# Kernel optimization log

Hardware: AMD Instinct MI355X
Metric: run time of the kernel (lower is better)

The kernel has to match this reference:

```python
import jax, jax.numpy as jnp
import numpy as np

N_NODES = 5000
K_POOL = 30
BN_EPS = 1e-5


def setup_inputs() -> dict:
    key = jax.random.key(0)
    ks = jax.random.split(key, 16)
    B, N, Din, C, H, OUT, E = 32, N_NODES, 16, 64, 128, 2, 80000
    F_tot = Din + 3 * C  # concat of input + 3 conv layers = 208
    return {
        "x": jax.random.normal(ks[0], (B, N, Din), jnp.float32),
        "age": jax.random.uniform(ks[1], (B,), jnp.float32) * 100.0,
        "edge_attr": jax.random.uniform(ks[2], (E,), jnp.float32) + 0.1,
        "W0": jax.random.normal(ks[3], (Din, C), jnp.float32) * 0.1,
        "b0": jnp.zeros((C,), jnp.float32),
        "W1": jax.random.normal(ks[4], (C, C), jnp.float32) * 0.1,
        "b1": jnp.zeros((C,), jnp.float32),
        "W2": jax.random.normal(ks[5], (C, C), jnp.float32) * 0.1,
        "b2": jnp.zeros((C,), jnp.float32),
        "g0": jnp.ones((C,), jnp.float32),
        "be0": jnp.zeros((C,), jnp.float32),
        "g1": jnp.ones((C,), jnp.float32),
        "be1": jnp.zeros((C,), jnp.float32),
        "mW0": jax.random.normal(ks[6], (K_POOL * F_tot + 1, H), jnp.float32) * 0.02,
        "mb0": jnp.zeros((H,), jnp.float32),
        "mW1": jax.random.normal(ks[7], (H, OUT), jnp.float32) * 0.1,
        "mb1": jnp.zeros((OUT,), jnp.float32),
        "edge_row": jax.random.randint(ks[8], (E,), 0, N, jnp.int32),
        "edge_col": jax.random.randint(ks[9], (E,), 0, N, jnp.int32),
    }


def _spmm(xw, rows, cols, nv):
    # xw: (B, N, C); out[b, r] = sum_{edges (r,c)} nv * xw[b, c]
    def one(xb):
        return jax.ops.segment_sum(xb[cols] * nv[:, None], rows, num_segments=N_NODES)
    return jax.vmap(one)(xw)


def reference(x, age, edge_attr, W0, b0, W1, b1, W2, b2, g0, be0, g1, be1,
              mW0, mb0, mW1, mb1, edge_row, edge_col):
    N = N_NODES
    # GCN normalization on A + I (gcn_norm with edge weights, self-loop value 1)
    loop = jnp.arange(N, dtype=edge_row.dtype)
    rows = jnp.concatenate([edge_row, loop])
    cols = jnp.concatenate([edge_col, loop])
    vals = jnp.concatenate([edge_attr, jnp.ones((N,), edge_attr.dtype)])
    deg = jax.ops.segment_sum(vals, rows, num_segments=N)
    dinv = jnp.where(deg > 0, jax.lax.rsqrt(jnp.maximum(deg, 1e-12)), 0.0)
    nv = dinv[rows] * vals * dinv[cols]

    feats = [x]
    h = x
    convs = [(W0, b0), (W1, b1), (W2, b2)]
    bns = [(g0, be0), (g1, be1)]
    for i, (W, b) in enumerate(convs):
        h = _spmm(h @ W, rows, cols, nv) + b  # GCNConv
        if i < len(convs) - 1:
            g, be = bns[i]
            mu = jnp.mean(h, axis=(0, 1))   # BatchNorm1d over flattened (B*N, C)
            var = jnp.var(h, axis=(0, 1))
            h = (h - mu) * jax.lax.rsqrt(var + BN_EPS) * g + be
        h = jax.nn.relu(h)  # dropout p=0.0 -> identity
        feats.append(h)

    z = jnp.concatenate(feats, axis=-1)  # (B, N, 208)
    # global_sort_pool: sort nodes by last feature channel, descending, take top-k
    order = jnp.argsort(-z[:, :, -1], axis=1)[:, :K_POOL]  # (B, k)
    zk = jnp.take_along_axis(z, order[:, :, None], axis=1)  # (B, k, 208)
    flat = zk.reshape(z.shape[0], -1)
    flat = jnp.concatenate([flat, age[:, None]], axis=1)  # append age scalar

    hm = jax.nn.relu(flat @ mW0 + mb0)  # MLP head
    out = hm @ mW1 + mb1
    return jax.nn.log_softmax(out, axis=-1)
```

## Files before the change

kernel.cpp:

```cpp
#include <hip/hip_runtime.h>
#include <math.h>

#define NN    5000
#define NE    80000
#define NB    32
#define DIN   16
#define CH    64
#define KPOOL 30
#define FTOT  208
#define FLATW 6241
#define NH    128
#define NG    8
#define GB    4
#define NPB   16
#define NCHUNK 313
#define NPAD  5008
#define NEPAD (NE + 4 * NN)
#define NSLOT 32



__global__ void k_init(float* deg, int* counts, float* stats, float* hm, int* perm) {
    int i = blockIdx.x * 256 + threadIdx.x;
    if (i < NN) { deg[i] = 1.0f; counts[i] = 0; }
    if (i < 2 * NSLOT * 128) stats[i] = 0.0f;
    if (i < 4096) hm[i] = 0.0f;
    if (i >= NN && i < NPAD) perm[i] = NN;
}

#define NEB 313
__global__ void k_edges(const float* __restrict__ attr, const int* __restrict__ erow,
                        float* deg, int* counts) {
    int e = blockIdx.x * 256 + threadIdx.x;
    if (e < NE) {
        int r = erow[e];
        atomicAdd(&deg[r], attr[e]);
        atomicAdd(&counts[r], 1);
    }
}

__global__ __launch_bounds__(1024) void k_phase1(
        const int* __restrict__ counts, const float* __restrict__ deg,
        int* rowptr, int* cursor, float* dinv, int* perm,
        const float* __restrict__ x, float* __restrict__ xt) {
    __shared__ int wsum[16], woff[16];
    __shared__ int carry_sh;
    __shared__ int hist[256];
    int t = threadIdx.x;
    if (blockIdx.x >= 2) {
        int idx = (blockIdx.x - 2) * 1024 + t;
        if (idx >= NB * NN) return;
        int b = idx / NN, n = idx % NN;
        int g4 = b >> 3, bi8 = b & 7;
        const float4* src = (const float4*)(x + (size_t)idx * DIN);
        float4* dst = (float4*)(xt + (((size_t)g4 * NN + n) * 8 + bi8) * DIN);
        dst[0] = src[0]; dst[1] = src[1]; dst[2] = src[2]; dst[3] = src[3];
        return;
    }
    if (blockIdx.x == 0) {
        int lane = t & 63, wid = t >> 6;
        if (t == 0) carry_sh = 0;
        __syncthreads();
        for (int base = 0; base < NN; base += 1024) {
            int carry = carry_sh;
            int i = base + t;
            int v = 0;
            if (i < NN) {
                v = (counts[i] + 3) & ~3;
                dinv[i] = 1.0f / sqrtf(deg[i]);
            }
            int s = v;
#pragma unroll
            for (int off = 1; off < 64; off <<= 1) {
                int o = __shfl_up(s, off);
                if (lane >= off) s += o;
            }
            if (lane == 63) wsum[wid] = s;
            __syncthreads();
            if (t < 16) {
                int w = wsum[t];
#pragma unroll
                for (int off = 1; off < 16; off <<= 1) {
                    int o = __shfl_up(w, off);
                    if (t >= off) w += o;
                }
                woff[t] = w;
            }
            __syncthreads();
            int inc = s + (wid > 0 ? woff[wid - 1] : 0) + carry;
            if (i < NN) {
                rowptr[i + 1] = inc;
                cursor[i] = inc - v;
            }
            if (t == 1023) carry_sh = carry + woff[15];
            __syncthreads();
        }
        if (t == 0) rowptr[0] = 0;
    } else {
        if (t < 256) hist[t] = 0;
        __syncthreads();
        for (int i = t; i < NN; i += 1024) {
            int b = 255 - min(((counts[i] + 3) & ~3) >> 2, 255);
            atomicAdd(&hist[b], 1);
        }
        __syncthreads();
        int mycnt = (t < 256) ? hist[t] : 0;
        for (int off = 1; off < 256; off <<= 1) {
            int v = (t < 256 && t >= off) ? hist[t - off] : 0;
            __syncthreads();
            if (t < 256) hist[t] += v;
            __syncthreads();
        }
        if (t < 256) hist[t] -= mycnt;
        __syncthreads();
        for (int i = t; i < NN; i += 1024) {
            int b = 255 - min(((counts[i] + 3) & ~3) >> 2, 255);
            int pos = atomicAdd(&hist[b], 1);
            perm[pos] = i;
        }
    }
}

__global__ __launch_bounds__(1024) void k_build(
        const int* __restrict__ erow, const int* __restrict__ ecol,
        const float* __restrict__ attr, const float* __restrict__ dinv,
        const int* __restrict__ counts, const int* __restrict__ rowptr,
        int* cursor, int* csr_col, float* csr_nv) {
    int t = blockIdx.x * 1024 + threadIdx.x;
    if (t < NE) {
        int r = erow[t], c = ecol[t];
        int pos = atomicAdd(&cursor[r], 1);
        csr_col[pos] = c;
        csr_nv[pos] = dinv[r] * attr[t] * dinv[c];
    } else if (t - NE < NN) {
        int i = t - NE;
        int cnt = counts[i];
        int pcnt = (cnt + 3) & ~3;
        int base = rowptr[i + 1] - pcnt;
        for (int p = base + cnt; p < base + pcnt; ++p) { csr_col[p] = i; csr_nv[p] = 0.0f; }
    }
}

__device__ __forceinline__ float4 actv(float4 v, float4 s, float4 t) {
    v.x = fmaxf(fmaf(v.x, s.x, t.x), 0.f);
    v.y = fmaxf(fmaf(v.y, s.y, t.y), 0.f);
    v.z = fmaxf(fmaf(v.z, s.z, t.z), 0.f);
    v.w = fmaxf(fmaf(v.w, s.w, t.w), 0.f);
    return v;
}
__device__ __forceinline__ void fma4(float4& a, float w, float4 v) {
    a.x = fmaf(w, v.x, a.x); a.y = fmaf(w, v.y, a.y);
    a.z = fmaf(w, v.z, a.z); a.w = fmaf(w, v.w, a.w);
}
__device__ __forceinline__ void fma2(float2& a, float w, float2 v) {
    a.x = fmaf(w, v.x, a.x); a.y = fmaf(w, v.y, a.y);
}

__global__ __launch_bounds__(256) void k_l16(
        const float* __restrict__ in,
        const float* __restrict__ W, const float* __restrict__ bias,
        const int* __restrict__ rowptr, const int* __restrict__ csr_col,
        const float* __restrict__ csr_nv, const float* __restrict__ dinv,
        const int* __restrict__ perm,
        float* __restrict__ out, float* __restrict__ stats) {
    const int ALS = 18;
    __shared__ float As[4 * 32 * ALS];
    int tid = threadIdx.x;
    int wid = tid >> 6, lane = tid & 63;
    int g4 = blockIdx.x & 3;
    int base = (blockIdx.x >> 2) * NPB + wid * 4;
    float* Aw = As + wid * 32 * ALS;
    const int4 pid = *(const int4*)(perm + base);

    const float2* __restrict__ in2 = (const float2*)in + (size_t)g4 * NN * 64;
    int bi8 = lane >> 3, chp = lane & 7;

#pragma unroll
    for (int pr = 0; pr < 2; ++pr) {
        int id0 = (pr == 0) ? pid.x : pid.z;
        int id1 = (pr == 0) ? pid.y : pid.w;
        bool vn0 = id0 < NN, vn1 = id1 < NN;
        int rc0 = vn0 ? id0 : 0, rc1 = vn1 ? id1 : 0;
        float dd0 = dinv[rc0]; dd0 *= dd0;
        float dd1 = dinv[rc1]; dd1 *= dd1;
        float2 a0 = {0.f, 0.f}, a1 = {0.f, 0.f};
        {
            float2 v0 = in2[(size_t)rc0 * 64 + lane];
            float2 v1 = in2[(size_t)rc1 * 64 + lane];
            if (vn0) { a0.x = dd0 * v0.x; a0.y = dd0 * v0.y; }
            if (vn1) { a1.x = dd1 * v1.x; a1.y = dd1 * v1.y; }
        }
        int p0a = rowptr[rc0], na = vn0 ? (rowptr[rc0 + 1] - p0a) >> 2 : 0;
        int p0b = rowptr[rc1], nbv = vn1 ? (rowptr[rc1 + 1] - p0b) >> 2 : 0;
        int mx = max(na, nbv);
        for (int bb = 0; bb < mx; ++bb) {
            int ea = min(p0a + 4 * bb, NEPAD - 4);
            int eb = min(p0b + 4 * bb, NEPAD - 4);
            bool va = bb < na, vb = bb < nbv;
            int4   ca = *(const int4*)(csr_col + ea);
            float4 wa = *(const float4*)(csr_nv + ea);
            int4   cb = *(const int4*)(csr_col + eb);
            float4 wb = *(const float4*)(csr_nv + eb);
            if (!va) { wa.x = 0.f; wa.y = 0.f; wa.z = 0.f; wa.w = 0.f;
                       ca.x = 0; ca.y = 0; ca.z = 0; ca.w = 0; }
            if (!vb) { wb.x = 0.f; wb.y = 0.f; wb.z = 0.f; wb.w = 0.f;
                       cb.x = 0; cb.y = 0; cb.z = 0; cb.w = 0; }
            float2 u0 = in2[(size_t)ca.x * 64 + lane];
            float2 u1 = in2[(size_t)ca.y * 64 + lane];
            float2 u2 = in2[(size_t)ca.z * 64 + lane];
            float2 u3 = in2[(size_t)ca.w * 64 + lane];
            float2 t0 = in2[(size_t)cb.x * 64 + lane];
            float2 t1 = in2[(size_t)cb.y * 64 + lane];
            float2 t2 = in2[(size_t)cb.z * 64 + lane];
            float2 t3 = in2[(size_t)cb.w * 64 + lane];
            fma2(a0, wa.x, u0);
            fma2(a0, wa.y, u1);
            fma2(a0, wa.z, u2);
            fma2(a0, wa.w, u3);
            fma2(a1, wb.x, t0);
            fma2(a1, wb.y, t1);
            fma2(a1, wb.z, t2);
            fma2(a1, wb.w, t3);
        }
        *(float2*)(Aw + ((2 * pr + 0) * 8 + bi8) * ALS + chp * 2) = a0;
        *(float2*)(Aw + ((2 * pr + 1) * 8 + bi8) * ALS + chp * 2) = a1;
    }

    int colq = lane & 15, rowq = lane >> 4;
    int node = (rowq == 0) ? pid.x : (rowq == 1) ? pid.y : (rowq == 2) ? pid.z : pid.w;

    const float4* __restrict__ W4 = (const float4*)W;
    float4 bb4 = ((const float4*)bias)[colq];
    float4 o[8];
#pragma unroll
    for (int i = 0; i < 8; ++i) o[i] = bb4;
#pragma unroll
    for (int k = 0; k < 16; ++k) {
        float4 w4 = W4[k * 16 + colq];
#pragma unroll
        for (int i = 0; i < 8; ++i)
            fma4(o[i], Aw[(rowq * 8 + i) * ALS + k], w4);
    }
    if (node < NN) {
#pragma unroll
        for (int i = 0; i < 8; ++i) {
            int g8 = g4 * 2 + (i >> 2);
            float4* op = (float4*)(out + (((size_t)g8 * NN + node) * 4 + (i & 3)) * 64);
            op[colq] = o[i];
        }
    }

    float4 s4 = {0,0,0,0}, q4 = {0,0,0,0};
    if (node < NN) {
#pragma unroll
        for (int i = 0; i < 8; ++i) {
            s4.x += o[i].x; s4.y += o[i].y; s4.z += o[i].z; s4.w += o[i].w;
            q4.x = fmaf(o[i].x, o[i].x, q4.x); q4.y = fmaf(o[i].y, o[i].y, q4.y);
            q4.z = fmaf(o[i].z, o[i].z, q4.z); q4.w = fmaf(o[i].w, o[i].w, q4.w);
        }
    }
    s4.x += __shfl_xor(s4.x, 16); s4.y += __shfl_xor(s4.y, 16);
    s4.z += __shfl_xor(s4.z, 16); s4.w += __shfl_xor(s4.w, 16);
    q4.x += __shfl_xor(q4.x, 16); q4.y += __shfl_xor(q4.y, 16);
    q4.z += __shfl_xor(q4.z, 16); q4.w += __shfl_xor(q4.w, 16);
    s4.x += __shfl_xor(s4.x, 32); s4.y += __shfl_xor(s4.y, 32);
    s4.z += __shfl_xor(s4.z, 32); s4.w += __shfl_xor(s4.w, 32);
    q4.x += __shfl_xor(q4.x, 32); q4.y += __shfl_xor(q4.y, 32);
    q4.z += __shfl_xor(q4.z, 32); q4.w += __shfl_xor(q4.w, 32);
    __syncthreads();
    if (lane < 16) {
        float* S = As + wid * 128;
        *(float4*)(S + lane * 8) = s4;
        *(float4*)(S + lane * 8 + 4) = q4;
    }
    __syncthreads();
    if (tid < 64) {
        int cq = tid >> 2, comp = tid & 3;
        float s = 0.f, q = 0.f;
#pragma unroll
        for (int w = 0; w < 4; ++w) {
            s += As[w * 128 + cq * 8 + comp];
            q += As[w * 128 + cq * 8 + 4 + comp];
        }
        float* sl = stats + (blockIdx.x & (NSLOT - 1)) * 128;
        atomicAdd(&sl[tid], s);
        atomicAdd(&sl[64 + tid], q);
    }
}

__global__ __launch_bounds__(256) void k_l64(
        const float* __restrict__ in, const float* __restrict__ bnstats,
        const float* __restrict__ gamma, const float* __restrict__ beta,
        const float* __restrict__ W, const float* __restrict__ bias,
        const int* __restrict__ rowptr, const int* __restrict__ csr_col,
        const float* __restrict__ csr_nv, const float* __restrict__ dinv,
        const int* __restrict__ perm,
        float* __restrict__ out, float* __restrict__ stats) {
    const int ALS = 68;
    __shared__ float As[4 * 16 * ALS];
    __shared__ float stl[128];
    int tid = threadIdx.x;
    int wid = tid >> 6, lane = tid & 63;
    int g = blockIdx.x & 7;
    int base = (blockIdx.x >> 3) * NPB + wid * 4;
    float* Aw = As + wid * 16 * ALS;
    const int4 pid = *(const int4*)(perm + base);

    if (tid < 64) {
        float su = 0.f, qu = 0.f;
#pragma unroll
        for (int s = 0; s < NSLOT; ++s) {
            su += bnstats[s * 128 + tid];
            qu += bnstats[s * 128 + 64 + tid];
        }
        const float inv = 1.0f / (float)(NB * NN);
        float mu = su * inv;
        float var = qu * inv - mu * mu;
        float sc = gamma[tid] / sqrtf(var + 1e-5f);
        stl[tid] = sc;
        stl[64 + tid] = fmaf(-mu, sc, beta[tid]);
    }
    __syncthreads();

    const float4* __restrict__ in4 = (const float4*)in + (size_t)g * NN * 64;
    int c4 = lane & 15, bi = lane >> 4;
    float4 sv = ((const float4*)stl)[c4];
    float4 tv = ((const float4*)(stl + 64))[c4];
#pragma unroll
    for (int pr = 0; pr < 2; ++pr) {
        int id0 = (pr == 0) ? pid.x : pid.z;
        int id1 = (pr == 0) ? pid.y : pid.w;
        bool vn0 = id0 < NN, vn1 = id1 < NN;
        int rc0 = vn0 ? id0 : 0, rc1 = vn1 ? id1 : 0;
        float dd0 = dinv[rc0]; dd0 *= dd0;
        float dd1 = dinv[rc1]; dd1 *= dd1;
        float4 a0 = {0.f,0.f,0.f,0.f}, a1 = {0.f,0.f,0.f,0.f};
        {
            float4 v0 = actv(in4[(size_t)rc0 * 64 + lane], sv, tv);
            float4 v1 = actv(in4[(size_t)rc1 * 64 + lane], sv, tv);
            if (vn0) { a0.x = dd0 * v0.x; a0.y = dd0 * v0.y; a0.z = dd0 * v0.z; a0.w = dd0 * v0.w; }
            if (vn1) { a1.x = dd1 * v1.x; a1.y = dd1 * v1.y; a1.z = dd1 * v1.z; a1.w = dd1 * v1.w; }
        }
        int p0a = rowptr[rc0], na = vn0 ? (rowptr[rc0 + 1] - p0a) >> 2 : 0;
        int p0b = rowptr[rc1], nbv = vn1 ? (rowptr[rc1 + 1] - p0b) >> 2 : 0;
        int mx = max(na, nbv);
        for (int bb = 0; bb < mx; ++bb) {
            int ea = min(p0a + 4 * bb, NEPAD - 4);
            int eb = min(p0b + 4 * bb, NEPAD - 4);
            bool va = bb < na, vb = bb < nbv;
            int4   ca = *(const int4*)(csr_col + ea);
            float4 wa = *(const float4*)(csr_nv + ea);
            int4   cb = *(const int4*)(csr_col + eb);
            float4 wb = *(const float4*)(csr_nv + eb);
            if (!va) { wa.x = 0.f; wa.y = 0.f; wa.z = 0.f; wa.w = 0.f;
                       ca.x = 0; ca.y = 0; ca.z = 0; ca.w = 0; }
            if (!vb) { wb.x = 0.f; wb.y = 0.f; wb.z = 0.f; wb.w = 0.f;
                       cb.x = 0; cb.y = 0; cb.z = 0; cb.w = 0; }
            float4 u0 = in4[(size_t)ca.x * 64 + lane];
            float4 u1 = in4[(size_t)ca.y * 64 + lane];
            float4 u2 = in4[(size_t)ca.z * 64 + lane];
            float4 u3 = in4[(size_t)ca.w * 64 + lane];
            float4 t0 = in4[(size_t)cb.x * 64 + lane];
            float4 t1 = in4[(size_t)cb.y * 64 + lane];
            float4 t2 = in4[(size_t)cb.z * 64 + lane];
            float4 t3 = in4[(size_t)cb.w * 64 + lane];
            fma4(a0, wa.x, actv(u0, sv, tv));
            fma4(a0, wa.y, actv(u1, sv, tv));
            fma4(a0, wa.z, actv(u2, sv, tv));
            fma4(a0, wa.w, actv(u3, sv, tv));
            fma4(a1, wb.x, actv(t0, sv, tv));
            fma4(a1, wb.y, actv(t1, sv, tv));
            fma4(a1, wb.z, actv(t2, sv, tv));
            fma4(a1, wb.w, actv(t3, sv, tv));
        }
        *(float4*)(Aw + ((pr * 2 + 0) * 4 + bi) * ALS + c4 * 4) = a0;
        *(float4*)(Aw + ((pr * 2 + 1) * 4 + bi) * ALS + c4 * 4) = a1;
    }

    int colq = lane & 15, rowq = lane >> 4;
    int node = (rowq == 0) ? pid.x : (rowq == 1) ? pid.y : (rowq == 2) ? pid.z : pid.w;

    const float4* __restrict__ W4 = (const float4*)W;
    float4 bb = ((const float4*)bias)[colq];
    float4 o[4];
#pragma unroll
    for (int i = 0; i < 4; ++i) o[i] = bb;
#pragma unroll 8
    for (int k = 0; k < 64; ++k) {
        float4 w4 = W4[k * 16 + colq];
#pragma unroll
        for (int i = 0; i < 4; ++i) {
            float a = Aw[(rowq * 4 + i) * ALS + k];
            fma4(o[i], a, w4);
        }
    }
    if (node < NN) {
        float4* __restrict__ op = (float4*)(out + ((size_t)g * NN + node) * 256);
#pragma unroll
        for (int i = 0; i < 4; ++i) op[i * 16 + colq] = o[i];
    }

    float4 s4 = {0,0,0,0}, q4 = {0,0,0,0};
    if (node < NN) {
#pragma unroll
        for (int i = 0; i < 4; ++i) {
            s4.x += o[i].x; s4.y += o[i].y; s4.z += o[i].z; s4.w += o[i].w;
            q4.x = fmaf(o[i].x, o[i].x, q4.x); q4.y = fmaf(o[i].y, o[i].y, q4.y);
            q4.z = fmaf(o[i].z, o[i].z, q4.z); q4.w = fmaf(o[i].w, o[i].w, q4.w);
        }
    }
    s4.x += __shfl_xor(s4.x, 16); s4.y += __shfl_xor(s4.y, 16);
    s4.z += __shfl_xor(s4.z, 16); s4.w += __shfl_xor(s4.w, 16);
    q4.x += __shfl_xor(q4.x, 16); q4.y += __shfl_xor(q4.y, 16);
    q4.z += __shfl_xor(q4.z, 16); q4.w += __shfl_xor(q4.w, 16);
    s4.x += __shfl_xor(s4.x, 32); s4.y += __shfl_xor(s4.y, 32);
    s4.z += __shfl_xor(s4.z, 32); s4.w += __shfl_xor(s4.w, 32);
    q4.x += __shfl_xor(q4.x, 32); q4.y += __shfl_xor(q4.y, 32);
    q4.z += __shfl_xor(q4.z, 32); q4.w += __shfl_xor(q4.w, 32);
    __syncthreads();
    if (lane < 16) {
        float* S = As + wid * 128;
        *(float4*)(S + lane * 8) = s4;
        *(float4*)(S + lane * 8 + 4) = q4;
    }
    __syncthreads();
    if (tid < 64) {
        int cq = tid >> 2, comp = tid & 3;
        float s = 0.f, q = 0.f;
#pragma unroll
        for (int w = 0; w < 4; ++w) {
            s += As[w * 128 + cq * 8 + comp];
            q += As[w * 128 + cq * 8 + 4 + comp];
        }
        float* sl = stats + (blockIdx.x & (NSLOT - 1)) * 128;
        atomicAdd(&sl[tid], s);
        atomicAdd(&sl[64 + tid], q);
    }
}

#define ZBLK 2048
__global__ __launch_bounds__(256) void k_z(
        const float* __restrict__ h2, const float* __restrict__ bnstats,
        const float* __restrict__ gamma, const float* __restrict__ beta,
        const float* __restrict__ W2, float* __restrict__ z) {
    __shared__ float stl[128];
    __shared__ float w63[64];
    int tid = threadIdx.x;
    if (tid < 64) {
        float su = 0.f, qu = 0.f;
#pragma unroll
        for (int s = 0; s < NSLOT; ++s) {
            su += bnstats[s * 128 + tid];
            qu += bnstats[s * 128 + 64 + tid];
        }
        const float inv = 1.0f / (float)(NB * NN);
        float mu = su * inv;
        float var = qu * inv - mu * mu;
        float sc = gamma[tid] / sqrtf(var + 1e-5f);
        stl[tid] = sc;
        stl[64 + tid] = fmaf(-mu, sc, beta[tid]);
        w63[tid] = W2[tid * 64 + 63];
    }
    __syncthreads();
    int lane = tid & 63, wid = tid >> 6;
    int c4 = lane & 15;
    float4 sv = ((const float4*)stl)[c4];
    float4 tv = ((const float4*)(stl + 64))[c4];
    float4 w4 = ((const float4*)w63)[c4];
    const int total = NB * NN;
    for (int base = blockIdx.x * 16; base < total; base += ZBLK * 16) {
        int row = base + wid * 4 + (lane >> 4);
        float s = 0.f;
        if (row < total) {
            float4 v = ((const float4*)h2)[(size_t)row * 16 + c4];
            v.x = fmaxf(fmaf(v.x, sv.x, tv.x), 0.f);
            v.y = fmaxf(fmaf(v.y, sv.y, tv.y), 0.f);
            v.z = fmaxf(fmaf(v.z, sv.z, tv.z), 0.f);
            v.w = fmaxf(fmaf(v.w, sv.w, tv.w), 0.f);
            s = v.x * w4.x + v.y * w4.y + v.z * w4.z + v.w * w4.w;
        }
        s += __shfl_xor(s, 1);
        s += __shfl_xor(s, 2);
        s += __shfl_xor(s, 4);
        s += __shfl_xor(s, 8);
        if ((lane & 15) == 0 && row < total) z[row] = s;
    }
}

__global__ __launch_bounds__(256) void k_score(
        const float* __restrict__ z, const float* __restrict__ b2,
        const int* __restrict__ rowptr, const int* __restrict__ csr_col,
        const float* __restrict__ csr_nv, const float* __restrict__ dinv,
        float* __restrict__ sc) {
    int tid = threadIdx.x;
    int wid = tid >> 6, lane = tid & 63;
    int g = blockIdx.x & 7;
    int nd = (blockIdx.x >> 3) * 4 + wid;
    if (nd >= NN) return;
    const float4* __restrict__ z4 = (const float4*)z + (size_t)g * NN;
    int p0 = rowptr[nd], p1 = rowptr[nd + 1];
    float4 a = {0.f, 0.f, 0.f, 0.f};
    for (int e = p0 + lane; e < p1; e += 64) {
        int col = csr_col[e];
        float nv = csr_nv[e];
        float4 zv = z4[col];
        fma4(a, nv, zv);
    }
#pragma unroll
    for (int off = 1; off < 64; off <<= 1) {
        a.x += __shfl_xor(a.x, off);
        a.y += __shfl_xor(a.y, off);
        a.z += __shfl_xor(a.z, off);
        a.w += __shfl_xor(a.w, off);
    }
    if (lane == 0) {
        float d = dinv[nd]; d *= d;
        float4 zs = z4[nd];
        float bb = b2[63];
        float4 o;
        o.x = fmaxf(fmaf(d, zs.x, a.x) + bb, 0.f);
        o.y = fmaxf(fmaf(d, zs.y, a.y) + bb, 0.f);
        o.z = fmaxf(fmaf(d, zs.z, a.z) + bb, 0.f);
        o.w = fmaxf(fmaf(d, zs.w, a.w) + bb, 0.f);
        ((float4*)sc)[(size_t)g * NN + nd] = o;
    }
}

__global__ __launch_bounds__(1024) void k_toppool(const float* __restrict__ sc, int* order,
        const float* __restrict__ stats,
        const float* __restrict__ g0, const float* __restrict__ be0,
        const float* __restrict__ g1, const float* __restrict__ be1,
        float* __restrict__ st) {
    __shared__ unsigned long long wbest[16];
    __shared__ unsigned long long winner;
    int tid = threadIdx.x;
    if (blockIdx.x == NB) {
        if (tid < 128) {
            int c = tid & 63, layer = tid >> 6;
            const float* sb = stats + layer * NSLOT * 128;
            float su = 0.f, qu = 0.f;
#pragma unroll
            for (int s = 0; s < NSLOT; ++s) {
                su += sb[s * 128 + c];
                qu += sb[s * 128 + 64 + c];
            }
            const float inv = 1.0f / (float)(NB * NN);
            float mu = su * inv;
            float var = qu * inv - mu * mu;
            float g = layer ? g1[c] : g0[c];
            float be = layer ? be1[c] : be0[c];
            float scv = g / sqrtf(var + 1e-5f);
            st[layer * 128 + c] = scv;
            st[layer * 128 + 64 + c] = fmaf(-mu, scv, be);
        }
        return;
    }
    int b = blockIdx.x;
    int g = b >> 2, bi = b & 3;
    int lane = tid & 63, wid = tid >> 6;
    unsigned long long key[5];
#pragma unroll
    for (int j = 0; j < 5; ++j) {
        int n = tid + j * 1024;
        unsigned long long k = 0;
        if (n < NN) {
            float v = sc[((size_t)g * NN + n) * GB + bi];
            k = ((unsigned long long)__float_as_uint(v) << 32) | (unsigned int)(NN - n);
        }
        key[j] = k;
    }
    for (int k = 0; k < KPOOL; ++k) {
        unsigned long long best = key[0];
#pragma unroll
        for (int j = 1; j < 5; ++j) best = (key[j] > best) ? key[j] : best;
#pragma unroll
        for (int off = 1; off < 64; off <<= 1) {
            unsigned long long o = __shfl_xor(best, off);
            best = (o > best) ? o : best;
        }
        if (lane == 0) wbest[wid] = best;
        __syncthreads();
        if (tid == 0) {
            unsigned long long w = wbest[0];
#pragma unroll
            for (int i = 1; i < 16; ++i) w = (wbest[i] > w) ? wbest[i] : w;
            winner = w;
            order[b * KPOOL + k] = NN - (int)(w & 0xFFFFFFFFu);
        }
        __syncthreads();
        int n = NN - (int)(winner & 0xFFFFFFFFu);
        if ((n & 1023) == tid) key[n >> 10] = 0;
    }
}

__global__ void k_gather(const float* __restrict__ xt, const float* __restrict__ h1,
                         const float* __restrict__ h2,
                         const float* __restrict__ W2, const float* __restrict__ b2,
                         const float* __restrict__ st, const float* __restrict__ age,
                         const int* __restrict__ rowptr, const int* __restrict__ csr_col,
                         const float* __restrict__ csr_nv, const float* __restrict__ dinv,
                         const int* __restrict__ order, float* __restrict__ flat) {
    __shared__ float aggP[4][64];
    __shared__ float aggRow[64];
    int bk = blockIdx.x;
    int b = bk / KPOOL, k = bk % KPOOL;
    int n = order[bk];
    int g = b >> 2, bi = b & 3;
    size_t node = (size_t)g * NN + n;
    int tid = threadIdx.x;
    {
        int ep = tid >> 6, c = tid & 63;
        float sc1 = st[128 + c], sh1 = st[192 + c];
        float a = 0.f;
        if (ep == 0) {
            float d = dinv[n];
            float v = h2[(node * GB + bi) * CH + c];
            a = d * d * fmaxf(fmaf(v, sc1, sh1), 0.f);
        }
        int p0 = rowptr[n], p1 = rowptr[n + 1];
        for (int e = p0 + ep; e < p1; e += 4) {
            int col = csr_col[e];
            float nv = csr_nv[e];
            float v = h2[(((size_t)g * NN + col) * GB + bi) * CH + c];
            a += nv * fmaxf(fmaf(v, sc1, sh1), 0.f);
        }
        aggP[ep][c] = a;
    }
    __syncthreads();
    if (tid < 64) aggRow[tid] = aggP[0][tid] + aggP[1][tid] + aggP[2][tid] + aggP[3][tid];
    __syncthreads();
    int f = tid;
    float val = 0.f;
    if (f < DIN) {
        val = xt[(((size_t)(b >> 3) * NN + n) * 8 + (b & 7)) * DIN + f];
    } else if (f < DIN + CH) {
        int c = f - DIN;
        val = fmaxf(fmaf(h1[(node * GB + bi) * CH + c], st[c], st[64 + c]), 0.f);
    } else if (f < DIN + 2 * CH) {
        int c = f - DIN - CH;
        val = fmaxf(fmaf(h2[(node * GB + bi) * CH + c], st[128 + c], st[192 + c]), 0.f);
    } else if (f < FTOT) {
        int c = f - DIN - 2 * CH;
        float s = b2[c];
#pragma unroll 8
        for (int kk = 0; kk < 64; ++kk)
            s = fmaf(aggRow[kk], W2[kk * 64 + c], s);
        val = fmaxf(s, 0.f);
    }
    if (f < FTOT) flat[(size_t)b * FLATW + k * FTOT + f] = val;
    if (bk == 0 && f >= FTOT && f < FTOT + NB)
        flat[(size_t)(f - FTOT) * FLATW + (FLATW - 1)] = age[f - FTOT];
}

__global__ void k_head1(const float* __restrict__ flat, const float* __restrict__ mW0,
                        float* hm) {
    int tid = threadIdx.x;
    int j4 = (tid & 31) * 4;
    int b0 = (tid >> 5) * 4;
    int kbase = blockIdx.x * 64;
    float acc[4][4];
#pragma unroll
    for (int i = 0; i < 4; i++)
#pragma unroll
        for (int jj = 0; jj < 4; jj++) acc[i][jj] = 0.f;
    int kend = FLATW - kbase; if (kend > 64) kend = 64;
    for (int kk = 0; kk < kend; ++kk) {
        int k = kbase + kk;
        float4 w = *(const float4*)(mW0 + (size_t)k * NH + j4);
#pragma unroll
        for (int i = 0; i < 4; i++) {
            float fv = flat[(size_t)(b0 + i) * FLATW + k];
            acc[i][0] = fmaf(fv, w.x, acc[i][0]);
            acc[i][1] = fmaf(fv, w.y, acc[i][1]);
            acc[i][2] = fmaf(fv, w.z, acc[i][2]);
            acc[i][3] = fmaf(fv, w.w, acc[i][3]);
        }
    }
#pragma unroll
    for (int i = 0; i < 4; i++)
#pragma unroll
        for (int jj = 0; jj < 4; jj++)
            atomicAdd(&hm[(size_t)(b0 + i) * NH + j4 + jj], acc[i][jj]);
}

__global__ void k_head2(const float* __restrict__ hm, const float* __restrict__ mb0,
                        const float* __restrict__ mW1, const float* __restrict__ mb1,
                        float* __restrict__ out) {
    __shared__ float part[256];
    __shared__ float vals[64];
    int tid = threadIdx.x;
    int q = tid & 3, o = (tid >> 2) & 1, b = tid >> 3;
    float acc = 0.f;
    for (int j = q * 32; j < q * 32 + 32; ++j) {
        float hv = fmaxf(hm[b * NH + j] + mb0[j], 0.f);
        acc = fmaf(hv, mW1[j * 2 + o], acc);
    }
    part[tid] = acc;
    __syncthreads();
    if (tid < 64) {
        int b2 = tid >> 1, o2 = tid & 1;
        int base = (b2 << 3) + (o2 << 2);
        vals[tid] = part[base] + part[base + 1] + part[base + 2] + part[base + 3] + mb1[o2];
    }
    __syncthreads();
    if (tid < 64) {
        int b2 = tid >> 1;
        float v0 = vals[b2 * 2], v1 = vals[b2 * 2 + 1];
        float m = fmaxf(v0, v1);
        float lse = m + logf(expf(v0 - m) + expf(v1 - m));
        out[tid] = vals[tid] - lse;
    }
}

extern "C" void kernel_launch(void* const* d_in, const int* in_sizes, int n_in,
                              void* d_out, int out_size, void* d_ws, size_t ws_size,
                              hipStream_t stream) {
    const float* x    = (const float*)d_in[0];
    const float* age  = (const float*)d_in[1];
    const float* attr = (const float*)d_in[2];
    const float* W0   = (const float*)d_in[3];
    const float* b0   = (const float*)d_in[4];
    const float* W1   = (const float*)d_in[5];
    const float* b1   = (const float*)d_in[6];
    const float* W2   = (const float*)d_in[7];
    const float* b2   = (const float*)d_in[8];
    const float* g0   = (const float*)d_in[9];
    const float* be0  = (const float*)d_in[10];
    const float* g1   = (const float*)d_in[11];
    const float* be1  = (const float*)d_in[12];
    const float* mW0  = (const float*)d_in[13];
    const float* mb0  = (const float*)d_in[14];
    const float* mW1  = (const float*)d_in[15];
    const float* mb1  = (const float*)d_in[16];
    const int* erow   = (const int*)d_in[17];
    const int* ecol   = (const int*)d_in[18];
    float* out = (float*)d_out;

    float* ws     = (float*)d_ws;
    float* deg    = ws;
    float* dinv   = deg + 5008;
    int*   counts = (int*)(dinv + 5008);
    int*   rowptr = counts + 5008;
    int*   cursor = rowptr + 5008;
    int*   perm   = cursor + 5008;
    int*   csr_col= perm + 5008;
    float* csr_nv = (float*)(csr_col + NEPAD);
    float* stats  = csr_nv + NEPAD;
    float* st     = stats + 2 * NSLOT * 128;
    float* sc     = st + 256;
    int*   order  = (int*)(sc + NB * NN);
    float* flat   = (float*)(order + 960);
    float* hm     = flat + (size_t)NB * FLATW;
    float* xt     = hm + 4096;
    float* h1     = xt + (size_t)NB * NN * DIN;
    float* h2     = h1 + (size_t)NB * NN * CH;
    float* z      = h2 + (size_t)NB * NN * CH;

    k_init<<<32, 256, 0, stream>>>(deg, counts, stats, hm, perm);
    k_edges<<<NEB, 256, 0, stream>>>(attr, erow, deg, counts);
    k_phase1<<<2 + (NB * NN + 1023) / 1024, 1024, 0, stream>>>(counts, deg, rowptr, cursor, dinv, perm, x, xt);
    k_build<<<(NE + NN + 1023) / 1024, 1024, 0, stream>>>(erow, ecol, attr, dinv, counts, rowptr, cursor, csr_col, csr_nv);

    k_l16<<<NCHUNK * 4, 256, 0, stream>>>(xt, W0, b0, rowptr, csr_col, csr_nv, dinv, perm, h1, stats);
    k_l64<<<NCHUNK * NG, 256, 0, stream>>>(h1, stats, g0, be0, W1, b1, rowptr, csr_col, csr_nv, dinv, perm, h2, stats + NSLOT * 128);
    k_z<<<ZBLK, 256, 0, stream>>>(h2, stats + NSLOT * 128, g1, be1, W2, z);
    k_score<<<(NN / 4) * NG, 256, 0, stream>>>(z, b2, rowptr, csr_col, csr_nv, dinv, sc);

    k_toppool<<<NB + 1, 1024, 0, stream>>>(sc, order, stats, g0, be0, g1, be1, st);
    k_gather<<<NB * KPOOL, 256, 0, stream>>>(xt, h1, h2, W2, b2, st, age, rowptr, csr_col, csr_nv, dinv, order, flat);
    k_head1<<<(FLATW + 63) / 64, 256, 0, stream>>>(flat, mW0, hm);
    k_head2<<<1, 256, 0, stream>>>(hm, mb0, mW1, mb1, out);
}
```

Before: 318.4 us.

## Compute per-wave top-k independently then merge candidates in one wave

Replaces the block-wide iterative argmax, which needed two __syncthreads per selected element, with per-wavefront top-k selection. Each wave writes its 30 candidates to shared memory, and a single wave then merges the 480 candidates into the global top-30. This cuts block barriers from 60 to 1 per batch element. In exchange, every wave now does 30 rounds of selection and the merge phase runs serially on one wave.

```diff
diff --git a/kernel.cpp b/kernel.cpp
--- a/kernel.cpp
+++ b/kernel.cpp
@@ -531,8 +531,7 @@
         const float* __restrict__ g0, const float* __restrict__ be0,
         const float* __restrict__ g1, const float* __restrict__ be1,
         float* __restrict__ st) {
-    __shared__ unsigned long long wbest[16];
-    __shared__ unsigned long long winner;
+    __shared__ unsigned long long cand[16 * KPOOL];
     int tid = threadIdx.x;
     if (blockIdx.x == NB) {
         if (tid < 128) {
@@ -578,18 +577,35 @@
             unsigned long long o = __shfl_xor(best, off);
             best = (o > best) ? o : best;
         }
-        if (lane == 0) wbest[wid] = best;
-        __syncthreads();
-        if (tid == 0) {
-            unsigned long long w = wbest[0];
-#pragma unroll
-            for (int i = 1; i < 16; ++i) w = (wbest[i] > w) ? wbest[i] : w;
-            winner = w;
-            order[b * KPOOL + k] = NN - (int)(w & 0xFFFFFFFFu);
-        }
-        __syncthreads();
-        int n = NN - (int)(winner & 0xFFFFFFFFu);
-        if ((n & 1023) == tid) key[n >> 10] = 0;
+        if (best) {
+#pragma unroll
+            for (int j = 0; j < 5; ++j) if (key[j] == best) key[j] = 0;
+        }
+        if (lane == 0) cand[wid * KPOOL + k] = best;
+    }
+    __syncthreads();
+    if (wid == 0) {
+        unsigned long long r[8];
+#pragma unroll
+        for (int i = 0; i < 8; ++i) {
+            int idx = i * 64 + lane;
+            r[i] = (idx < 16 * KPOOL) ? cand[idx] : 0;
+        }
+        for (int k = 0; k < KPOOL; ++k) {
+            unsigned long long best = r[0];
+#pragma unroll
+            for (int i = 1; i < 8; ++i) best = (r[i] > best) ? r[i] : best;
+#pragma unroll
+            for (int off = 1; off < 64; off <<= 1) {
+                unsigned long long o = __shfl_xor(best, off);
+                best = (o > best) ? o : best;
+            }
+            if (best) {
+#pragma unroll
+                for (int i = 0; i < 8; ++i) if (r[i] == best) r[i] = 0;
+            }
+            if (lane == 0) order[b * KPOOL + k] = NN - (int)(best & 0xFFFFFFFFu);
+        }
     }
 }
 
```

Result: no change. 317.2 us (-0.4%).
